# Optimization experiments

Measured on AMD Instinct MI355X. Metric: run time of the kernel, lower is better.

## Reference

```python
import jax, jax.numpy as jnp
import numpy as np

B, LQ, D_MODEL, H, L_CACHE, WINDOW = 4, 512, 2048, 16, 4096, 4096
D_HEAD = D_MODEL // H
EPS = 1e-8


def setup_inputs() -> dict:
    key = jax.random.key(0)
    ks = jax.random.split(key, 9)
    x_chunk = jax.random.normal(ks[0], (B, LQ, D_MODEL), dtype=jnp.float32)
    # int8-range cache values stored as int32 in [-127, 128)
    k_q = jax.random.randint(ks[1], (B, H, L_CACHE, D_HEAD), 0, 255, dtype=jnp.int32) - 127
    v_q = jax.random.randint(ks[2], (B, H, L_CACHE, D_HEAD), 0, 255, dtype=jnp.int32) - 127
    # per-position scales, typical magnitude amax/127
    k_s = jax.random.uniform(ks[3], (B, H, L_CACHE, 1), dtype=jnp.float32, minval=0.005, maxval=0.03)
    v_s = jax.random.uniform(ks[4], (B, H, L_CACHE, 1), dtype=jnp.float32, minval=0.005, maxval=0.03)
    s = 1.0 / np.sqrt(D_MODEL)
    W_q = jax.random.normal(ks[5], (D_MODEL, D_MODEL), dtype=jnp.float32) * s
    W_k = jax.random.normal(ks[6], (D_MODEL, D_MODEL), dtype=jnp.float32) * s
    W_v = jax.random.normal(ks[7], (D_MODEL, D_MODEL), dtype=jnp.float32) * s
    W_o = jax.random.normal(ks[8], (D_MODEL, D_MODEL), dtype=jnp.float32) * s
    return {"x_chunk": x_chunk, "k_q": k_q, "v_q": v_q, "k_s": k_s, "v_s": v_s,
            "W_q": W_q, "W_k": W_k, "W_v": W_v, "W_o": W_o, "window_size": WINDOW}


def _split_heads(x):  # (B, L, d_model) -> (B, H, L, d_head)
    Bb, L, _ = x.shape
    return x.reshape(Bb, L, H, D_HEAD).transpose(0, 2, 1, 3)


def _merge_heads(x):  # (B, H, L, d_head) -> (B, L, d_model)
    Bb, Hh, L, dh = x.shape
    return x.transpose(0, 2, 1, 3).reshape(Bb, L, Hh * dh)


def quantize_int8_lastdim(x):
    amax = jnp.max(jnp.abs(x), axis=-1, keepdims=True)
    scale = jnp.maximum(amax / 127.0, EPS)
    q = jnp.clip(jnp.round(x / scale), -127, 127).astype(jnp.int8)
    return q, scale.astype(jnp.float16)


def reference(x_chunk, k_q, v_q, k_s, v_s, W_q, W_k, W_v, W_o, window_size):
    Lq = x_chunk.shape[1]
    scale = 1.0 / np.sqrt(D_HEAD)
    q = _split_heads(x_chunk @ W_q.T)
    k_new = _split_heads(x_chunk @ W_k.T)
    v_new = _split_heads(x_chunk @ W_v.T)
    # dequantize int8 KV cache: q * scale (per position)
    k_cache = k_q.astype(jnp.float32) * k_s.astype(jnp.float32)
    v_cache = v_q.astype(jnp.float32) * v_s.astype(jnp.float32)
    k_total = jnp.concatenate([k_cache, k_new], axis=2)  # (B,H,Lk,dh)
    v_total = jnp.concatenate([v_cache, v_new], axis=2)
    Lk_total = k_total.shape[2]
    L_cache = k_cache.shape[2]
    # chunked causal mask with cache offset: key j visible to query i iff j <= L_cache + i
    i = jnp.arange(Lq)[:, None]
    j = jnp.arange(Lk_total)[None, :]
    mask = j > (L_cache + i)  # (Lq, Lk)
    attn = jnp.einsum('bhqd,bhkd->bhqk', q, k_total) * scale
    attn = jnp.where(mask[None, None], jnp.finfo(attn.dtype).min, attn)
    attn = jax.nn.softmax(attn, axis=-1)
    y = jnp.einsum('bhqk,bhkd->bhqd', attn, v_total)
    y = _merge_heads(y) @ W_o.T  # (B, Lq, d_model)
    # sliding-window truncation of cache, then re-quantize
    if Lk_total > window_size:
        k_total = k_total[:, :, -window_size:, :]
        v_total = v_total[:, :, -window_size:, :]
    k_tq, k_scale = quantize_int8_lastdim(k_total)
    v_tq, v_scale = quantize_int8_lastdim(v_total)
    return y, k_tq, v_tq, k_scale, v_scale
```

## Files before the change

### kernel.cpp

```cpp
#include <hip/hip_runtime.h>
#include <hip/hip_fp16.h>

typedef float   f32x4   __attribute__((ext_vector_type(4)));
typedef float   f32x2   __attribute__((ext_vector_type(2)));
typedef float   f32x16  __attribute__((ext_vector_type(16)));
typedef short   short8v __attribute__((ext_vector_type(8)));
typedef unsigned short ushort8v __attribute__((ext_vector_type(8)));
typedef unsigned int   u32x4v __attribute__((ext_vector_type(4)));
typedef unsigned int   u32x2v __attribute__((ext_vector_type(2)));
typedef int     int2v   __attribute__((ext_vector_type(2)));
typedef int     int4v   __attribute__((ext_vector_type(4)));
typedef unsigned int   u32;
typedef unsigned short u16;

#define DEVI static __device__ __forceinline__

DEVI u16 f2bf(float f) {
    u32 u = __builtin_bit_cast(u32, f);
    u += 0x7FFFu + ((u >> 16) & 1u);
    return (u16)(u >> 16);
}
DEVI float bf2f(u16 h) { return __builtin_bit_cast(float, (u32)h << 16); }

DEVI void gl_lds16(const u16* g, u16* l) {
    __builtin_amdgcn_global_load_lds(
        (const __attribute__((address_space(1))) u32*)(const void*)g,
        (__attribute__((address_space(3))) u32*)(void*)l, 16, 0, 0);
}

__global__ __launch_bounds__(256) void convert_kernel(
    const float* __restrict__ src, u16* __restrict__ dst, float scale, int n8) {
    int idx = blockIdx.x * 256 + threadIdx.x;
    if (idx >= n8) return;
    const float* p = src + (size_t)idx * 8;
    f32x4 a = *(const f32x4*)p, b = *(const f32x4*)(p + 4);
    ushort8v o;
    o[0]=f2bf(a[0]*scale); o[1]=f2bf(a[1]*scale); o[2]=f2bf(a[2]*scale); o[3]=f2bf(a[3]*scale);
    o[4]=f2bf(b[0]*scale); o[5]=f2bf(b[1]*scale); o[6]=f2bf(b[2]*scale); o[7]=f2bf(b[3]*scale);
    *(ushort8v*)(dst + (size_t)idx * 8) = o;
}

__global__ __launch_bounds__(256) void convert4_kernel(
    const float* __restrict__ x, const float* __restrict__ Wq,
    const float* __restrict__ Wk, const float* __restrict__ Wv,
    u16* __restrict__ xb, u16* __restrict__ wb3, float rscale) {
    const int seg = blockIdx.x >> 11;
    const int idx = (blockIdx.x & 2047) * 256 + threadIdx.x;
    const float* src; u16* dst; float scale = 1.0f;
    if (seg == 0)      { src = x;  dst = xb; }
    else if (seg == 1) { src = Wq; dst = wb3; scale = rscale; }
    else if (seg == 2) { src = Wk; dst = wb3 + 4194304; }
    else               { src = Wv; dst = wb3 + 8388608; }
    const float* p = src + (size_t)idx * 8;
    f32x4 a = *(const f32x4*)p, b = *(const f32x4*)(p + 4);
    ushort8v o;
    o[0]=f2bf(a[0]*scale); o[1]=f2bf(a[1]*scale); o[2]=f2bf(a[2]*scale); o[3]=f2bf(a[3]*scale);
    o[4]=f2bf(b[0]*scale); o[5]=f2bf(b[1]*scale); o[6]=f2bf(b[2]*scale); o[7]=f2bf(b[3]*scale);
    *(ushort8v*)(dst + (size_t)idx * 8) = o;
}

DEVI void prep_body(int pid, char* LB,
    const int* __restrict__ kq, const int* __restrict__ vq,
    const float* __restrict__ ks, const float* __restrict__ vs,
    u16* __restrict__ kcb, u16* __restrict__ vt,
    float* __restrict__ oktq, float* __restrict__ ovtq,
    float* __restrict__ oksc, float* __restrict__ ovsc) {
    u16 (*Vs)[132] = (u16(*)[132])LB;
    float* skL = (float*)(LB + 16896);
    float* svL = (float*)(LB + 17152);
    const int tid = threadIdx.x;
    const int bh = pid >> 6, kt = pid & 63;
    const int key0 = kt << 6;
    const size_t rowbase = (size_t)bh * 4096 + key0;
    if (tid < 64) { skL[tid] = ks[rowbase + tid]; svL[tid] = vs[rowbase + tid]; }
    __syncthreads();
    const int lane = tid & 63, w = tid >> 6;
    const int q31 = lane & 31, rh = lane >> 5;
    u32x2v* kcw = (u32x2v*)kcb;
    #pragma unroll 4
    for (int s = 0; s < 8; ++s) {
        const int key = s * 8 + w * 2 + rh;
        const size_t row = rowbase + key;
        const float sk = skL[key], sv = svL[key];
        int4v kv = *(const int4v*)(kq + row * 128 + q31 * 4);
        int4v vv = *(const int4v*)(vq + row * 128 + q31 * 4);
        f32x4 kx, vx;
        #pragma unroll
        for (int e = 0; e < 4; ++e) { kx[e] = (float)kv[e] * sk; vx[e] = (float)vv[e] * sv; }
        u32x2v kp, vp;
        kp[0] = (u32)f2bf(kx[0]) | ((u32)f2bf(kx[1]) << 16);
        kp[1] = (u32)f2bf(kx[2]) | ((u32)f2bf(kx[3]) << 16);
        vp[0] = (u32)f2bf(vx[0]) | ((u32)f2bf(vx[1]) << 16);
        vp[1] = (u32)f2bf(vx[2]) | ((u32)f2bf(vx[3]) << 16);
        kcw[(size_t)(bh * 4608 + key0 + key) * 32 + q31] = kp;
        *(u32x2v*)&Vs[key][q31 * 4] = vp;
        float kam = fmaxf(fmaxf(fabsf(kx[0]), fabsf(kx[1])), fmaxf(fabsf(kx[2]), fabsf(kx[3])));
        float vam = fmaxf(fmaxf(fabsf(vx[0]), fabsf(vx[1])), fmaxf(fabsf(vx[2]), fabsf(vx[3])));
        #pragma unroll
        for (int off = 1; off < 32; off <<= 1) {
            kam = fmaxf(kam, __shfl_xor(kam, off, 64));
            vam = fmaxf(vam, __shfl_xor(vam, off, 64));
        }
        const int r = key0 + key;
        if (r >= 512) {
            const size_t orow = (size_t)bh * 4096 + (size_t)(r - 512);
            float kscale = fmaxf(kam / 127.0f, 1e-8f);
            float vscale = fmaxf(vam / 127.0f, 1e-8f);
            float kinv = 1.0f / kscale, vinv = 1.0f / vscale;
            f32x4 ko, vo;
            #pragma unroll
            for (int e = 0; e < 4; ++e) {
                ko[e] = fminf(fmaxf(rintf(kx[e] * kinv), -127.f), 127.f);
                vo[e] = fminf(fmaxf(rintf(vx[e] * vinv), -127.f), 127.f);
            }
            *(f32x4*)(oktq + orow * 128 + q31 * 4) = ko;
            *(f32x4*)(ovtq + orow * 128 + q31 * 4) = vo;
            if (q31 == 0) {
                oksc[orow] = __half2float(__float2half(kscale));
                ovsc[orow] = __half2float(__float2half(vscale));
            }
        }
    }
    __syncthreads();
    const int d = tid >> 1, half = tid & 1;
    u16* obase = vt + ((size_t)bh * 128 + d) * 4608 + key0 + half * 32;
    #pragma unroll
    for (int c = 0; c < 4; ++c) {
        ushort8v tv;
        #pragma unroll
        for (int e = 0; e < 8; ++e) tv[e] = Vs[half * 32 + c * 8 + e][d];
        *(ushort8v*)(obase + c * 8) = tv;
    }
}

DEVI void qkv_body(int qid, char* LB,
    const u16* __restrict__ A, const u16* __restrict__ Bw,
    u16* __restrict__ qbf, u16* __restrict__ kcb, u16* __restrict__ vnb) {
    u16* As = (u16*)LB;
    u16* Bs = (u16*)(LB + 32768);
    const int tid = threadIdx.x, lane = tid & 63, w = tid >> 6;
    const int sid = (qid & 7) * 192 + (qid >> 3);
    const int bm = sid & 15, bn = sid >> 4;
    const int m0 = bm * 128, n0 = bn * 64;
    const int wm = (w >> 1) * 64, wn = (w & 1) * 32;
    const int r16 = lane & 15, kb = lane >> 4;

    f32x4 acc[4][2] = {};

    auto stage = [&](int bi, int k0) {
        #pragma unroll
        for (int i = 0; i < 4; ++i) {
            int s = i * 256 + tid;
            int row = s >> 3, l = (s & 7) ^ (row & 7);
            gl_lds16(A + (size_t)(m0 + row) * 2048 + k0 + l * 8,
                     &As[bi * 8192 + (i * 256 + (tid & ~63)) * 8]);
        }
        #pragma unroll
        for (int i = 0; i < 2; ++i) {
            int s = i * 256 + tid;
            int row = s >> 3, l = (s & 7) ^ (row & 7);
            gl_lds16(Bw + (size_t)(n0 + row) * 2048 + k0 + l * 8,
                     &Bs[bi * 4096 + (i * 256 + (tid & ~63)) * 8]);
        }
    };

    stage(0, 0);
    __syncthreads();
    int cur = 0;
    for (int t = 0; t < 32; ++t) {
        if (t < 31) stage(cur ^ 1, (t + 1) * 64);
        short8v af[4][2], bf[2][2];
        #pragma unroll
        for (int mf = 0; mf < 4; ++mf) {
            int row = wm + mf * 16 + r16;
            #pragma unroll
            for (int ksv = 0; ksv < 2; ++ksv) {
                int blk = (ksv * 4 + kb) ^ (row & 7);
                af[mf][ksv] = __builtin_bit_cast(short8v,
                    *(const ushort8v*)&As[cur * 8192 + row * 64 + blk * 8]);
            }
        }
        #pragma unroll
        for (int nf = 0; nf < 2; ++nf) {
            int row = wn + nf * 16 + r16;
            #pragma unroll
            for (int ksv = 0; ksv < 2; ++ksv) {
                int blk = (ksv * 4 + kb) ^ (row & 7);
                bf[nf][ksv] = __builtin_bit_cast(short8v,
                    *(const ushort8v*)&Bs[cur * 4096 + row * 64 + blk * 8]);
            }
        }
        #pragma unroll
        for (int mf = 0; mf < 4; ++mf)
            #pragma unroll
            for (int nf = 0; nf < 2; ++nf)
                #pragma unroll
                for (int ksv = 0; ksv < 2; ++ksv)
                    acc[mf][nf] = __builtin_amdgcn_mfma_f32_16x16x32_bf16(
                        af[mf][ksv], bf[nf][ksv], acc[mf][nf], 0, 0, 0);
        __syncthreads();
        cur ^= 1;
    }

    #pragma unroll
    for (int mf = 0; mf < 4; ++mf)
        #pragma unroll
        for (int nf = 0; nf < 2; ++nf)
            #pragma unroll
            for (int v = 0; v < 4; ++v) {
                int mg = m0 + wm + mf * 16 + kb * 4 + v;
                int ng = n0 + wn + nf * 16 + r16;
                int nb = ng >> 11, ngl = ng & 2047;
                u16 val = f2bf(acc[mf][nf][v]);
                if (nb == 1) {
                    size_t bh = (size_t)(mg >> 9) * 16 + (ngl >> 7);
                    kcb[(bh * 4608 + 4096 + (mg & 511)) * 128 + (ngl & 127)] = val;
                } else {
                    u16* dst = (nb == 0) ? qbf : vnb;
                    dst[(((size_t)(mg >> 9) * 16 + (ngl >> 7)) * 512 +
                         (mg & 511)) * 128 + (ngl & 127)] = val;
                }
            }
}

__global__ __launch_bounds__(256, 3) void fused_prep_qkv_kernel(
    const int* __restrict__ kq, const int* __restrict__ vq,
    const float* __restrict__ ks, const float* __restrict__ vs,
    u16* __restrict__ kcb, u16* __restrict__ vt,
    float* __restrict__ oktq, float* __restrict__ ovtq,
    float* __restrict__ oksc, float* __restrict__ ovsc,
    const u16* __restrict__ xb, const u16* __restrict__ wb3,
    u16* __restrict__ qbf, u16* __restrict__ vnb) {
    __shared__ __align__(16) char LB[49152];
    const int grp = blockIdx.x / 11, rem = blockIdx.x % 11;
    if (rem < 8) {
        prep_body(grp * 8 + rem, LB, kq, vq, ks, vs, kcb, vt,
                  oktq, ovtq, oksc, ovsc);
    } else {
        qkv_body(grp * 3 + (rem - 8), LB, xb, wb3, qbf, kcb, vnb);
    }
}

__global__ __launch_bounds__(256) void gemm_wo_kernel(
    const u16* __restrict__ A, const u16* __restrict__ Bw,
    float* __restrict__ Cout) {
    __shared__ u16 As[2][128 * 64];
    __shared__ u16 Bs[2][64 * 64];
    const int tid = threadIdx.x, lane = tid & 63, w = tid >> 6;
    const int sid = (blockIdx.x & 7) * 64 + (blockIdx.x >> 3);
    const int bm = sid & 15, bn = sid >> 4;
    const int m0 = bm * 128, n0 = bn * 64;
    const int wm = (w >> 1) * 64, wn = (w & 1) * 32;
    const int r16 = lane & 15, kb = lane >> 4;

    f32x4 acc[4][2] = {};

    auto stage = [&](int bi, int k0) {
        #pragma unroll
        for (int i = 0; i < 4; ++i) {
            int s = i * 256 + tid;
            int row = s >> 3, l = (s & 7) ^ (row & 7);
            gl_lds16(A + (size_t)(m0 + row) * 2048 + k0 + l * 8,
                     &As[bi][(i * 256 + (tid & ~63)) * 8]);
        }
        #pragma unroll
        for (int i = 0; i < 2; ++i) {
            int s = i * 256 + tid;
            int row = s >> 3, l = (s & 7) ^ (row & 7);
            gl_lds16(Bw + (size_t)(n0 + row) * 2048 + k0 + l * 8,
                     &Bs[bi][(i * 256 + (tid & ~63)) * 8]);
        }
    };

    stage(0, 0);
    __syncthreads();
    int cur = 0;
    for (int t = 0; t < 32; ++t) {
        if (t < 31) stage(cur ^ 1, (t + 1) * 64);
        short8v af[4][2], bf[2][2];
        #pragma unroll
        for (int mf = 0; mf < 4; ++mf) {
            int row = wm + mf * 16 + r16;
            #pragma unroll
            for (int ksv = 0; ksv < 2; ++ksv) {
                int blk = (ksv * 4 + kb) ^ (row & 7);
                af[mf][ksv] = __builtin_bit_cast(short8v,
                    *(const ushort8v*)&As[cur][row * 64 + blk * 8]);
            }
        }
        #pragma unroll
        for (int nf = 0; nf < 2; ++nf) {
            int row = wn + nf * 16 + r16;
            #pragma unroll
            for (int ksv = 0; ksv < 2; ++ksv) {
                int blk = (ksv * 4 + kb) ^ (row & 7);
                bf[nf][ksv] = __builtin_bit_cast(short8v,
                    *(const ushort8v*)&Bs[cur][row * 64 + blk * 8]);
            }
        }
        #pragma unroll
        for (int mf = 0; mf < 4; ++mf)
            #pragma unroll
            for (int nf = 0; nf < 2; ++nf)
                #pragma unroll
                for (int ksv = 0; ksv < 2; ++ksv)
                    acc[mf][nf] = __builtin_amdgcn_mfma_f32_16x16x32_bf16(
                        af[mf][ksv], bf[nf][ksv], acc[mf][nf], 0, 0, 0);
        __syncthreads();
        cur ^= 1;
    }

    #pragma unroll
    for (int mf = 0; mf < 4; ++mf)
        #pragma unroll
        for (int nf = 0; nf < 2; ++nf)
            #pragma unroll
            for (int v = 0; v < 4; ++v) {
                int mg = m0 + wm + mf * 16 + kb * 4 + v;
                int ng = n0 + wn + nf * 16 + r16;
                Cout[(size_t)mg * 2048 + ng] = acc[mf][nf][v];
            }
}

__global__ __launch_bounds__(256) void quant_new_kernel(
    const u16* __restrict__ kcb, const u16* __restrict__ vnb,
    u16* __restrict__ vt,
    float* __restrict__ oktq, float* __restrict__ ovtq,
    float* __restrict__ oksc, float* __restrict__ ovsc) {
    __shared__ u16 Vs[64][132];
    const int tid = threadIdx.x;
    const int bh = blockIdx.x >> 3, kt = blockIdx.x & 7;
    const int i0 = kt << 6;
    const int lane = tid & 63, w = tid >> 6;
    const int q31 = lane & 31, rh = lane >> 5;
    #pragma unroll 4
    for (int s = 0; s < 8; ++s) {
        const int key = s * 8 + w * 2 + rh;
        const int i = i0 + key;
        u32x2v ku = *(const u32x2v*)(kcb + ((size_t)bh * 4608 + 4096 + i) * 128 + q31 * 4);
        u32x2v vu = *(const u32x2v*)(vnb + ((size_t)bh * 512 + i) * 128 + q31 * 4);
        f32x4 kx, vx;
        kx[0] = bf2f((u16)ku[0]); kx[1] = bf2f((u16)(ku[0] >> 16));
        kx[2] = bf2f((u16)ku[1]); kx[3] = bf2f((u16)(ku[1] >> 16));
        vx[0] = bf2f((u16)vu[0]); vx[1] = bf2f((u16)(vu[0] >> 16));
        vx[2] = bf2f((u16)vu[1]); vx[3] = bf2f((u16)(vu[1] >> 16));
        *(u32x2v*)&Vs[key][q31 * 4] = vu;
        float kam = fmaxf(fmaxf(fabsf(kx[0]), fabsf(kx[1])), fmaxf(fabsf(kx[2]), fabsf(kx[3])));
        float vam = fmaxf(fmaxf(fabsf(vx[0]), fabsf(vx[1])), fmaxf(fabsf(vx[2]), fabsf(vx[3])));
        #pragma unroll
        for (int off = 1; off < 32; off <<= 1) {
            kam = fmaxf(kam, __shfl_xor(kam, off, 64));
            vam = fmaxf(vam, __shfl_xor(vam, off, 64));
        }
        float kscale = fmaxf(kam / 127.0f, 1e-8f);
        float vscale = fmaxf(vam / 127.0f, 1e-8f);
        float kinv = 1.0f / kscale, vinv = 1.0f / vscale;
        const size_t orow = (size_t)bh * 4096 + 3584 + i;
        f32x4 ko, vo;
        #pragma unroll
        for (int e = 0; e < 4; ++e) {
            ko[e] = fminf(fmaxf(rintf(kx[e] * kinv), -127.f), 127.f);
            vo[e] = fminf(fmaxf(rintf(vx[e] * vinv), -127.f), 127.f);
        }
        *(f32x4*)(oktq + orow * 128 + q31 * 4) = ko;
        *(f32x4*)(ovtq + orow * 128 + q31 * 4) = vo;
        if (q31 == 0) {
            oksc[orow] = __half2float(__float2half(kscale));
            ovsc[orow] = __half2float(__float2half(vscale));
        }
    }
    __syncthreads();
    const int d = tid >> 1, half = tid & 1;
    u16* obase = vt + ((size_t)bh * 128 + d) * 4608 + 4096 + i0 + half * 32;
    #pragma unroll
    for (int c = 0; c < 4; ++c) {
        ushort8v tv;
        #pragma unroll
        for (int e = 0; e < 8; ++e) tv[e] = Vs[half * 32 + c * 8 + e][d];
        *(ushort8v*)(obase + c * 8) = tv;
    }
}

__global__ __launch_bounds__(256, 2) void attn_kernel(
    const u16* __restrict__ qb, const u16* __restrict__ kcb,
    const u16* __restrict__ vt, u16* __restrict__ Op0, u16* __restrict__ Op1,
    float* __restrict__ mlp) {
    __shared__ u16 Ks[2][64 * 128];
    __shared__ u16 Vl[2][128 * 64];

    const int tid = threadIdx.x, lane = tid & 63, w = tid >> 6;
    const int p = blockIdx.x;
    const int xcd = p & 7, i = p >> 3;
    const int qt2 = i & 3, sp = (i >> 2) & 1;
    const int bh = ((i >> 3) << 3) | xcd;
    const int q31 = lane & 31, hi = lane >> 5;
    const int qrow = qt2 * 128 + w * 32 + q31;

    const u16* qp = qb + ((size_t)bh * 512 + qrow) * 128 + hi * 8;
    short8v qf[8];
    #pragma unroll
    for (int s = 0; s < 8; ++s)
        qf[s] = __builtin_bit_cast(short8v, *(const ushort8v*)(qp + s * 16));

    f32x16 O[4] = {};
    float m_i = -3.0e38f, l_i = 0.f;

    const size_t kbase = (size_t)bh * 4608 * 128;
    const size_t vbase = (size_t)bh * 128 * 4608;
    const int ktA = sp ? 32 : 0;
    const int ktB = sp ? (66 + 2 * qt2) : 32;

    auto STAGE = [&](int bi, int kt) {
        #pragma unroll
        for (int ii = 0; ii < 4; ++ii) {
            int s = ii * 256 + tid;
            int row = s >> 4, l = (s & 15) ^ (row & 7);
            gl_lds16(kcb + kbase + (size_t)(kt * 64 + row) * 128 + l * 8,
                     &Ks[bi][(ii * 256 + (tid & ~63)) * 8]);
        }
        #pragma unroll
        for (int ii = 0; ii < 4; ++ii) {
            int s = ii * 256 + tid;
            int row = s >> 3, l = (s & 7) ^ (row & 7);
            gl_lds16(vt + vbase + (size_t)row * 4608 + kt * 64 + l * 8,
                     &Vl[bi][(ii * 256 + (tid & ~63)) * 8]);
        }
    };

    STAGE(0, ktA);
    __syncthreads();
    int cur = 0;
    for (int kt = ktA; kt < ktB; ++kt) {
        if (kt + 1 < ktB) STAGE(cur ^ 1, kt + 1);

        f32x16 S[2] = {};
        __builtin_amdgcn_s_setprio(1);
        #pragma unroll
        for (int s = 0; s < 8; ++s) {
            #pragma unroll
            for (int t = 0; t < 2; ++t) {
                int krow = t * 32 + q31;
                int blk = (2 * s + hi) ^ (krow & 7);
                short8v kf = __builtin_bit_cast(short8v,
                    *(const ushort8v*)&Ks[cur][krow * 128 + blk * 8]);
                S[t] = __builtin_amdgcn_mfma_f32_32x32x16_bf16(kf, qf[s], S[t], 0, 0, 0);
            }
        }
        __builtin_amdgcn_s_setprio(0);

        if (kt >= 64) {
            const int kb0 = (kt - 64) * 64 + 4 * hi;
            #pragma unroll
            for (int r = 0; r < 16; ++r) {
                int koff = kb0 + (r & 3) + 8 * (r >> 2);
                if (koff > qrow)      S[0][r] = -3.0e38f;
                if (koff + 32 > qrow) S[1][r] = -3.0e38f;
            }
        }

        float mx = fmaxf(S[0][0], S[1][0]);
        #pragma unroll
        for (int r = 1; r < 16; ++r) mx = fmaxf(mx, fmaxf(S[0][r], S[1][r]));
        mx = fmaxf(mx, __shfl_xor(mx, 32, 64));

        if (__ballot(mx > m_i + 8.f)) {
            float mnew = fmaxf(m_i, mx);
            float alpha = __expf(m_i - mnew);
            m_i = mnew;
            l_i *= alpha;
            #pragma unroll
            for (int r = 0; r < 16; ++r) {
                float ar = __shfl(alpha, (r & 3) + 8 * (r >> 2) + 4 * hi, 64);
                O[0][r] *= ar; O[1][r] *= ar; O[2][r] *= ar; O[3][r] *= ar;
            }
        }
        #pragma unroll
        for (int r = 0; r < 16; ++r) {
            S[0][r] = __expf(S[0][r] - m_i); l_i += S[0][r];
            S[1][r] = __expf(S[1][r] - m_i); l_i += S[1][r];
        }

        __builtin_amdgcn_s_setprio(1);
        #pragma unroll
        for (int j = 0; j < 4; ++j) {
            const int t = j >> 1, r0 = 8 * (j & 1);
            u32 a0, a1, b0, b1;
            asm("v_cvt_pk_bf16_f32 %0, %1, %2" : "=v"(a0) : "v"(S[t][r0+0]), "v"(S[t][r0+1]));
            asm("v_cvt_pk_bf16_f32 %0, %1, %2" : "=v"(a1) : "v"(S[t][r0+2]), "v"(S[t][r0+3]));
            asm("v_cvt_pk_bf16_f32 %0, %1, %2" : "=v"(b0) : "v"(S[t][r0+4]), "v"(S[t][r0+5]));
            asm("v_cvt_pk_bf16_f32 %0, %1, %2" : "=v"(b1) : "v"(S[t][r0+6]), "v"(S[t][r0+7]));
            asm("v_permlane32_swap_b32 %0, %1" : "+v"(a0), "+v"(b0));
            asm("v_permlane32_swap_b32 %0, %1" : "+v"(a1), "+v"(b1));
            u32x4v pw = {a0, a1, b0, b1};
            short8v pf = __builtin_bit_cast(short8v, pw);
            #pragma unroll
            for (int od = 0; od < 4; ++od) {
                int vrow = od * 32 + q31;
                int blk = (2 * j + hi) ^ (vrow & 7);
                short8v vf = __builtin_bit_cast(short8v,
                    *(const ushort8v*)&Vl[cur][vrow * 64 + blk * 8]);
                O[od] = __builtin_amdgcn_mfma_f32_32x32x16_bf16(pf, vf, O[od], 0, 0, 0);
            }
        }
        __builtin_amdgcn_s_setprio(0);

        __syncthreads();
        cur ^= 1;
    }

    float lt = l_i + __shfl_xor(l_i, 32, 64);
    u16* Op = sp ? Op1 : Op0;
    const size_t pbase = ((size_t)bh * 4 + qt2) * 16384;
    #pragma unroll
    for (int r = 0; r < 16; ++r) {
        int qoff = (r & 3) + 8 * (r >> 2) + 4 * hi;
        size_t rowb = pbase + (size_t)(w * 32 + qoff) * 128 + q31;
        Op[rowb +  0] = f2bf(O[0][r]);
        Op[rowb + 32] = f2bf(O[1][r]);
        Op[rowb + 64] = f2bf(O[2][r]);
        Op[rowb + 96] = f2bf(O[3][r]);
    }
    if (hi == 0) {
        int qg = ((sp * 256 + bh * 4 + qt2) * 128 + w * 32 + q31);
        mlp[qg * 2 + 0] = m_i;
        mlp[qg * 2 + 1] = lt;
    }
}

__global__ __launch_bounds__(256) void combine_kernel(
    const u16* __restrict__ Op0, const u16* __restrict__ Op1,
    const float* __restrict__ mlp, u16* __restrict__ yb) {
    const int p = blockIdx.x;
    const int bh = p >> 2, qt2 = p & 3;
    const int b = bh >> 4, h = bh & 15;
    const int q = threadIdx.x >> 1, dh = threadIdx.x & 1;
    const int base = (bh * 4 + qt2) * 128 + q;
    float m0 = mlp[base * 2], l0 = mlp[base * 2 + 1];
    float m1 = mlp[(256 * 128 + base) * 2], l1 = mlp[(256 * 128 + base) * 2 + 1];
    float M = fmaxf(m0, m1);
    float a0 = __expf(m0 - M), a1 = __expf(m1 - M);
    float invL = 1.0f / (l0 * a0 + l1 * a1);
    a0 *= invL; a1 *= invL;
    const size_t pb = ((size_t)bh * 4 + qt2) * 16384 + (size_t)q * 128 + dh * 64;
    u16* dst = yb + ((size_t)(b * 512 + qt2 * 128 + q)) * 2048 + h * 128 + dh * 64;
    #pragma unroll
    for (int j = 0; j < 8; ++j) {
        ushort8v o0 = *(const ushort8v*)(Op0 + pb + j * 8);
        ushort8v o1 = *(const ushort8v*)(Op1 + pb + j * 8);
        ushort8v o;
        #pragma unroll
        for (int e = 0; e < 8; ++e)
            o[e] = f2bf(bf2f(o0[e]) * a0 + bf2f(o1[e]) * a1);
        *(ushort8v*)(dst + j * 8) = o;
    }
}

extern "C" void kernel_launch(void* const* d_in, const int* in_sizes, int n_in,
                              void* d_out, int out_size, void* d_ws, size_t ws_size,
                              hipStream_t stream) {
    (void)in_sizes; (void)n_in; (void)out_size; (void)ws_size;
    const float* x   = (const float*)d_in[0];
    const int*   kq  = (const int*)d_in[1];
    const int*   vq  = (const int*)d_in[2];
    const float* ks  = (const float*)d_in[3];
    const float* vs  = (const float*)d_in[4];
    const float* Wq  = (const float*)d_in[5];
    const float* Wk  = (const float*)d_in[6];
    const float* Wv  = (const float*)d_in[7];
    const float* Wo  = (const float*)d_in[8];

    float* out  = (float*)d_out;
    float* y_o  = out;
    float* oktq = out + 4194304;
    float* ovtq = out + 37748736;
    float* oksc = out + 71303168;
    float* ovsc = out + 71565312;
    float* mlp  = out;

    char* wsb = (char*)d_ws;
    u16* kcb = (u16*)(wsb);
    u16* vtb = (u16*)(wsb + 75497472);
    u16* xb  = (u16*)(wsb + 150994944);
    u16* qbf = (u16*)(wsb + 159383552);
    u16* vnb = (u16*)(wsb + 167772160);
    u16* ybf = (u16*)(wsb + 176160768);
    u16* wb3 = (u16*)(wsb + 184549376);

    const float rscale = 0.08838834764831845f;
    const int n8 = 2048 * 2048 / 8;

    convert4_kernel<<<8192, 256, 0, stream>>>(x, Wq, Wk, Wv, xb, wb3, rscale);
    fused_prep_qkv_kernel<<<5632, 256, 0, stream>>>(
        kq, vq, ks, vs, kcb, vtb, oktq, ovtq, oksc, ovsc,
        xb, wb3, qbf, vnb);
    quant_new_kernel<<<512, 256, 0, stream>>>(kcb, vnb, vtb,
                                              oktq, ovtq, oksc, ovsc);
    attn_kernel<<<512, 256, 0, stream>>>(qbf, kcb, vtb, xb, vnb, mlp);
    combine_kernel<<<256, 256, 0, stream>>>(xb, vnb, mlp, ybf);
    convert_kernel<<<2048, 256, 0, stream>>>(Wo, wb3, 1.0f, n8);
    gemm_wo_kernel<<<512, 256, 0, stream>>>(ybf, wb3, y_o);
}
```

Baseline: 419.4 us.

## Split attention KV range three ways with smaller key tiles, batch prep loads

The attention kernel now splits each query tile's key range across three blocks instead of two, using 32-key tiles so LDS use drops and three blocks can share a CU. The combine kernel merges three partial softmax results, and workspace buffers are reassigned to hold the extra partial. The prep and quant_new kernels also issue all eight row loads before processing them, to expose more memory-level parallelism. The costs are more partial-output traffic, a heavier combine step, and per-tile overhead from the smaller key tiles.

New measurement: 411.4 us. About the same (-1.9%).

```diff
diff --git a/kernel.cpp b/kernel.cpp
--- a/kernel.cpp
+++ b/kernel.cpp
@@ -77,16 +77,22 @@
     const int lane = tid & 63, w = tid >> 6;
     const int q31 = lane & 31, rh = lane >> 5;
     u32x2v* kcw = (u32x2v*)kcb;
-    #pragma unroll 4
+
+    int4v kvr[8], vvr[8];
+    #pragma unroll
     for (int s = 0; s < 8; ++s) {
         const int key = s * 8 + w * 2 + rh;
         const size_t row = rowbase + key;
+        kvr[s] = *(const int4v*)(kq + row * 128 + q31 * 4);
+        vvr[s] = *(const int4v*)(vq + row * 128 + q31 * 4);
+    }
+    #pragma unroll
+    for (int s = 0; s < 8; ++s) {
+        const int key = s * 8 + w * 2 + rh;
         const float sk = skL[key], sv = svL[key];
-        int4v kv = *(const int4v*)(kq + row * 128 + q31 * 4);
-        int4v vv = *(const int4v*)(vq + row * 128 + q31 * 4);
         f32x4 kx, vx;
         #pragma unroll
-        for (int e = 0; e < 4; ++e) { kx[e] = (float)kv[e] * sk; vx[e] = (float)vv[e] * sv; }
+        for (int e = 0; e < 4; ++e) { kx[e] = (float)kvr[s][e] * sk; vx[e] = (float)vvr[s][e] * sv; }
         u32x2v kp, vp;
         kp[0] = (u32)f2bf(kx[0]) | ((u32)f2bf(kx[1]) << 16);
         kp[1] = (u32)f2bf(kx[2]) | ((u32)f2bf(kx[3]) << 16);
@@ -333,18 +339,25 @@
     const int i0 = kt << 6;
     const int lane = tid & 63, w = tid >> 6;
     const int q31 = lane & 31, rh = lane >> 5;
-    #pragma unroll 4
+
+    u32x2v kur[8], vur[8];
+    #pragma unroll
     for (int s = 0; s < 8; ++s) {
         const int key = s * 8 + w * 2 + rh;
         const int i = i0 + key;
-        u32x2v ku = *(const u32x2v*)(kcb + ((size_t)bh * 4608 + 4096 + i) * 128 + q31 * 4);
-        u32x2v vu = *(const u32x2v*)(vnb + ((size_t)bh * 512 + i) * 128 + q31 * 4);
+        kur[s] = *(const u32x2v*)(kcb + ((size_t)bh * 4608 + 4096 + i) * 128 + q31 * 4);
+        vur[s] = *(const u32x2v*)(vnb + ((size_t)bh * 512 + i) * 128 + q31 * 4);
+    }
+    #pragma unroll
+    for (int s = 0; s < 8; ++s) {
+        const int key = s * 8 + w * 2 + rh;
+        const int i = i0 + key;
         f32x4 kx, vx;
-        kx[0] = bf2f((u16)ku[0]); kx[1] = bf2f((u16)(ku[0] >> 16));
-        kx[2] = bf2f((u16)ku[1]); kx[3] = bf2f((u16)(ku[1] >> 16));
-        vx[0] = bf2f((u16)vu[0]); vx[1] = bf2f((u16)(vu[0] >> 16));
-        vx[2] = bf2f((u16)vu[1]); vx[3] = bf2f((u16)(vu[1] >> 16));
-        *(u32x2v*)&Vs[key][q31 * 4] = vu;
+        kx[0] = bf2f((u16)kur[s][0]); kx[1] = bf2f((u16)(kur[s][0] >> 16));
+        kx[2] = bf2f((u16)kur[s][1]); kx[3] = bf2f((u16)(kur[s][1] >> 16));
+        vx[0] = bf2f((u16)vur[s][0]); vx[1] = bf2f((u16)(vur[s][0] >> 16));
+        vx[2] = bf2f((u16)vur[s][1]); vx[3] = bf2f((u16)(vur[s][1] >> 16));
+        *(u32x2v*)&Vs[key][q31 * 4] = vur[s];
         float kam = fmaxf(fmaxf(fabsf(kx[0]), fabsf(kx[1])), fmaxf(fabsf(kx[2]), fabsf(kx[3])));
         float vam = fmaxf(fmaxf(fabsf(vx[0]), fabsf(vx[1])), fmaxf(fabsf(vx[2]), fabsf(vx[3])));
         #pragma unroll
@@ -381,18 +394,19 @@
     }
 }
 
-__global__ __launch_bounds__(256, 2) void attn_kernel(
+__global__ __launch_bounds__(256, 3) void attn_kernel(
     const u16* __restrict__ qb, const u16* __restrict__ kcb,
-    const u16* __restrict__ vt, u16* __restrict__ Op0, u16* __restrict__ Op1,
+    const u16* __restrict__ vt,
+    u16* __restrict__ Op0, u16* __restrict__ Op1, u16* __restrict__ Op2,
     float* __restrict__ mlp) {
-    __shared__ u16 Ks[2][64 * 128];
-    __shared__ u16 Vl[2][128 * 64];
+    __shared__ u16 Ks[2][32 * 128];
+    __shared__ u16 Vl[2][128 * 32];
 
     const int tid = threadIdx.x, lane = tid & 63, w = tid >> 6;
     const int p = blockIdx.x;
     const int xcd = p & 7, i = p >> 3;
-    const int qt2 = i & 3, sp = (i >> 2) & 1;
-    const int bh = ((i >> 3) << 3) | xcd;
+    const int qt2 = i & 3, spw = (i >> 2) % 3;
+    const int bh = ((i / 12) << 3) | xcd;
     const int q31 = lane & 31, hi = lane >> 5;
     const int qrow = qt2 * 128 + w * 32 + q31;
 
@@ -407,22 +421,23 @@
 
     const size_t kbase = (size_t)bh * 4608 * 128;
     const size_t vbase = (size_t)bh * 128 * 4608;
-    const int ktA = sp ? 32 : 0;
-    const int ktB = sp ? (66 + 2 * qt2) : 32;
+    const int e = 132 + 4 * qt2;
+    const int ktA = (e * spw) / 3;
+    const int ktB = (e * (spw + 1)) / 3;
 
     auto STAGE = [&](int bi, int kt) {
         #pragma unroll
-        for (int ii = 0; ii < 4; ++ii) {
+        for (int ii = 0; ii < 2; ++ii) {
             int s = ii * 256 + tid;
             int row = s >> 4, l = (s & 15) ^ (row & 7);
-            gl_lds16(kcb + kbase + (size_t)(kt * 64 + row) * 128 + l * 8,
+            gl_lds16(kcb + kbase + (size_t)(kt * 32 + row) * 128 + l * 8,
                      &Ks[bi][(ii * 256 + (tid & ~63)) * 8]);
         }
         #pragma unroll
-        for (int ii = 0; ii < 4; ++ii) {
+        for (int ii = 0; ii < 2; ++ii) {
             int s = ii * 256 + tid;
-            int row = s >> 3, l = (s & 7) ^ (row & 7);
-            gl_lds16(vt + vbase + (size_t)row * 4608 + kt * 64 + l * 8,
+            int row = s >> 2, l = (s & 3) ^ (row & 3);
+            gl_lds16(vt + vbase + (size_t)row * 4608 + kt * 32 + l * 8,
                      &Vl[bi][(ii * 256 + (tid & ~63)) * 8]);
         }
     };
@@ -433,34 +448,29 @@
     for (int kt = ktA; kt < ktB; ++kt) {
         if (kt + 1 < ktB) STAGE(cur ^ 1, kt + 1);
 
-        f32x16 S[2] = {};
+        f32x16 S = {};
         __builtin_amdgcn_s_setprio(1);
         #pragma unroll
         for (int s = 0; s < 8; ++s) {
-            #pragma unroll
-            for (int t = 0; t < 2; ++t) {
-                int krow = t * 32 + q31;
-                int blk = (2 * s + hi) ^ (krow & 7);
-                short8v kf = __builtin_bit_cast(short8v,
-                    *(const ushort8v*)&Ks[cur][krow * 128 + blk * 8]);
-                S[t] = __builtin_amdgcn_mfma_f32_32x32x16_bf16(kf, qf[s], S[t], 0, 0, 0);
-            }
+            int blk = (2 * s + hi) ^ (q31 & 7);
+            short8v kf = __builtin_bit_cast(short8v,
+                *(const ushort8v*)&Ks[cur][q31 * 128 + blk * 8]);
+            S = __builtin_amdgcn_mfma_f32_32x32x16_bf16(kf, qf[s], S, 0, 0, 0);
         }
         __builtin_amdgcn_s_setprio(0);
 
-        if (kt >= 64) {
-            const int kb0 = (kt - 64) * 64 + 4 * hi;
+        if (kt >= 128) {
+            const int kb0 = (kt - 128) * 32 + 4 * hi;
             #pragma unroll
             for (int r = 0; r < 16; ++r) {
                 int koff = kb0 + (r & 3) + 8 * (r >> 2);
-                if (koff > qrow)      S[0][r] = -3.0e38f;
-                if (koff + 32 > qrow) S[1][r] = -3.0e38f;
-            }
-        }
-
-        float mx = fmaxf(S[0][0], S[1][0]);
-        #pragma unroll
-        for (int r = 1; r < 16; ++r) mx = fmaxf(mx, fmaxf(S[0][r], S[1][r]));
+                if (koff > qrow) S[r] = -3.0e38f;
+            }
+        }
+
+        float mx = S[0];
+        #pragma unroll
+        for (int r = 1; r < 16; ++r) mx = fmaxf(mx, S[r]);
         mx = fmaxf(mx, __shfl_xor(mx, 32, 64));
 
         if (__ballot(mx > m_i + 8.f)) {
@@ -476,19 +486,18 @@
         }
         #pragma unroll
         for (int r = 0; r < 16; ++r) {
-            S[0][r] = __expf(S[0][r] - m_i); l_i += S[0][r];
-            S[1][r] = __expf(S[1][r] - m_i); l_i += S[1][r];
+            S[r] = __expf(S[r] - m_i); l_i += S[r];
         }
 
         __builtin_amdgcn_s_setprio(1);
         #pragma unroll
-        for (int j = 0; j < 4; ++j) {
-            const int t = j >> 1, r0 = 8 * (j & 1);
+        for (int j = 0; j < 2; ++j) {
+            const int r0 = 8 * j;
             u32 a0, a1, b0, b1;
-            asm("v_cvt_pk_bf16_f32 %0, %1, %2" : "=v"(a0) : "v"(S[t][r0+0]), "v"(S[t][r0+1]));
-            asm("v_cvt_pk_bf16_f32 %0, %1, %2" : "=v"(a1) : "v"(S[t][r0+2]), "v"(S[t][r0+3]));
-            asm("v_cvt_pk_bf16_f32 %0, %1, %2" : "=v"(b0) : "v"(S[t][r0+4]), "v"(S[t][r0+5]));
-            asm("v_cvt_pk_bf16_f32 %0, %1, %2" : "=v"(b1) : "v"(S[t][r0+6]), "v"(S[t][r0+7]));
+            asm("v_cvt_pk_bf16_f32 %0, %1, %2" : "=v"(a0) : "v"(S[r0+0]), "v"(S[r0+1]));
+            asm("v_cvt_pk_bf16_f32 %0, %1, %2" : "=v"(a1) : "v"(S[r0+2]), "v"(S[r0+3]));
+            asm("v_cvt_pk_bf16_f32 %0, %1, %2" : "=v"(b0) : "v"(S[r0+4]), "v"(S[r0+5]));
+            asm("v_cvt_pk_bf16_f32 %0, %1, %2" : "=v"(b1) : "v"(S[r0+6]), "v"(S[r0+7]));
             asm("v_permlane32_swap_b32 %0, %1" : "+v"(a0), "+v"(b0));
             asm("v_permlane32_swap_b32 %0, %1" : "+v"(a1), "+v"(b1));
             u32x4v pw = {a0, a1, b0, b1};
@@ -496,9 +505,9 @@
             #pragma unroll
             for (int od = 0; od < 4; ++od) {
                 int vrow = od * 32 + q31;
-                int blk = (2 * j + hi) ^ (vrow & 7);
+                int blk = (2 * j + hi) ^ (vrow & 3);
                 short8v vf = __builtin_bit_cast(short8v,
-                    *(const ushort8v*)&Vl[cur][vrow * 64 + blk * 8]);
+                    *(const ushort8v*)&Vl[cur][vrow * 32 + blk * 8]);
                 O[od] = __builtin_amdgcn_mfma_f32_32x32x16_bf16(pf, vf, O[od], 0, 0, 0);
             }
         }
@@ -509,7 +518,7 @@
     }
 
     float lt = l_i + __shfl_xor(l_i, 32, 64);
-    u16* Op = sp ? Op1 : Op0;
+    u16* Op = (spw == 0) ? Op0 : ((spw == 1) ? Op1 : Op2);
     const size_t pbase = ((size_t)bh * 4 + qt2) * 16384;
     #pragma unroll
     for (int r = 0; r < 16; ++r) {
@@ -521,7 +530,7 @@
         Op[rowb + 96] = f2bf(O[3][r]);
     }
     if (hi == 0) {
-        int qg = ((sp * 256 + bh * 4 + qt2) * 128 + w * 32 + q31);
+        int qg = ((spw * 256 + bh * 4 + qt2) * 128 + w * 32 + q31);
         mlp[qg * 2 + 0] = m_i;
         mlp[qg * 2 + 1] = lt;
     }
@@ -529,28 +538,31 @@
 
 __global__ __launch_bounds__(256) void combine_kernel(
     const u16* __restrict__ Op0, const u16* __restrict__ Op1,
+    const u16* __restrict__ Op2,
     const float* __restrict__ mlp, u16* __restrict__ yb) {
     const int p = blockIdx.x;
     const int bh = p >> 2, qt2 = p & 3;
     const int b = bh >> 4, h = bh & 15;
     const int q = threadIdx.x >> 1, dh = threadIdx.x & 1;
     const int base = (bh * 4 + qt2) * 128 + q;
-    float m0 = mlp[base * 2], l0 = mlp[base * 2 + 1];
-    float m1 = mlp[(256 * 128 + base) * 2], l1 = mlp[(256 * 128 + base) * 2 + 1];
-    float M = fmaxf(m0, m1);
-    float a0 = __expf(m0 - M), a1 = __expf(m1 - M);
-    float invL = 1.0f / (l0 * a0 + l1 * a1);
-    a0 *= invL; a1 *= invL;
+    float m0 = mlp[base * 2],               l0 = mlp[base * 2 + 1];
+    float m1 = mlp[(32768 + base) * 2],     l1 = mlp[(32768 + base) * 2 + 1];
+    float m2 = mlp[(65536 + base) * 2],     l2 = mlp[(65536 + base) * 2 + 1];
+    float M = fmaxf(fmaxf(m0, m1), m2);
+    float a0 = __expf(m0 - M), a1 = __expf(m1 - M), a2 = __expf(m2 - M);
+    float invL = 1.0f / (l0 * a0 + l1 * a1 + l2 * a2);
+    a0 *= invL; a1 *= invL; a2 *= invL;
     const size_t pb = ((size_t)bh * 4 + qt2) * 16384 + (size_t)q * 128 + dh * 64;
     u16* dst = yb + ((size_t)(b * 512 + qt2 * 128 + q)) * 2048 + h * 128 + dh * 64;
     #pragma unroll
     for (int j = 0; j < 8; ++j) {
         ushort8v o0 = *(const ushort8v*)(Op0 + pb + j * 8);
         ushort8v o1 = *(const ushort8v*)(Op1 + pb + j * 8);
+        ushort8v o2 = *(const ushort8v*)(Op2 + pb + j * 8);
         ushort8v o;
         #pragma unroll
         for (int e = 0; e < 8; ++e)
-            o[e] = f2bf(bf2f(o0[e]) * a0 + bf2f(o1[e]) * a1);
+            o[e] = f2bf(bf2f(o0[e]) * a0 + bf2f(o1[e]) * a1 + bf2f(o2[e]) * a2);
         *(ushort8v*)(dst + j * 8) = o;
     }
 }
@@ -595,8 +607,8 @@
         xb, wb3, qbf, vnb);
     quant_new_kernel<<<512, 256, 0, stream>>>(kcb, vnb, vtb,
                                               oktq, ovtq, oksc, ovsc);
-    attn_kernel<<<512, 256, 0, stream>>>(qbf, kcb, vtb, xb, vnb, mlp);
-    combine_kernel<<<256, 256, 0, stream>>>(xb, vnb, mlp, ybf);
+    attn_kernel<<<768, 256, 0, stream>>>(qbf, kcb, vtb, xb, vnb, ybf, mlp);
+    combine_kernel<<<256, 256, 0, stream>>>(xb, vnb, ybf, mlp, qbf);
     convert_kernel<<<2048, 256, 0, stream>>>(Wo, wb3, 1.0f, n8);
-    gemm_wo_kernel<<<512, 256, 0, stream>>>(ybf, wb3, y_o);
-}
+    gemm_wo_kernel<<<512, 256, 0, stream>>>(qbf, wb3, y_o);
+}
```
